# Kernel optimization log

Measured on AMD Instinct MI355X. Metric: run time of the kernel, lower is better.

Reference implementation:

```python
import jax, jax.numpy as jnp
import numpy as np

T, B, D = 1024, 64, 256   # time, batch, input dim
L, DC = 1024, 256         # context length, context dim
H, A = 256, 256           # hidden, attention dim
NEG = -1e9


def setup_inputs() -> dict:
    key = jax.random.key(0)
    ks = jax.random.split(key, 12)
    s = lambda fan: 1.0 / np.sqrt(fan)
    inp = {
        'x': jax.random.normal(ks[0], (T, B, D), jnp.float32),
        'lengths': jnp.maximum(jax.random.randint(ks[1], (B,), 1, T + 1), 1).astype(jnp.int32),
        'context': jax.random.normal(ks[2], (B, L, DC), jnp.float32),
        'ctx_lengths': jnp.maximum(jax.random.randint(ks[3], (B,), 1, L + 1), 1).astype(jnp.int32),
        'Wc': jax.random.normal(ks[4], (DC, A), jnp.float32) * s(DC),
        'Wx': jax.random.normal(ks[5], (D, A), jnp.float32) * s(D),
        'Wh': jax.random.normal(ks[6], (H, A), jnp.float32) * s(H),
        'v': jax.random.normal(ks[7], (A,), jnp.float32) * s(A),
        'W_ih': jax.random.normal(ks[8], (D + DC, 3 * H), jnp.float32) * s(D + DC),
        'W_hh': jax.random.normal(ks[9], (H, 3 * H), jnp.float32) * s(H),
        'b_ih': jnp.zeros((3 * H,), jnp.float32),
        'b_hh': jnp.zeros((3 * H,), jnp.float32),
    }
    return inp


def reference(x, lengths, context, ctx_lengths, Wc, Wx, Wh, v, W_ih, W_hh, b_ih, b_hh):
    # Precompute context projection once (shared across all timesteps). [B, L, A]
    ctx_proj = jnp.einsum('bld,da->bla', context, Wc)
    ctx_mask = jnp.arange(L)[None, :] < ctx_lengths[:, None]  # [B, L]
    h0 = jnp.zeros((B, H), x.dtype)

    def step(h, inputs):
        xt, t = inputs  # xt: [B, D]
        # Additive attention over the context.
        e = jnp.tanh(ctx_proj + (xt @ Wx)[:, None, :] + (h @ Wh)[:, None, :])  # [B, L, A]
        scores = jnp.where(ctx_mask, jnp.einsum('bla,a->bl', e, v), NEG)
        alpha = jax.nn.softmax(scores, axis=-1)                  # [B, L]
        c = jnp.einsum('bl,bld->bd', alpha, context)             # [B, DC]
        # GRU over [x_t ; c_t].
        z = jnp.concatenate([xt, c], axis=-1)                    # [B, D+DC]
        gi = z @ W_ih + b_ih
        gh = h @ W_hh + b_hh
        r = jax.nn.sigmoid(gi[:, :H] + gh[:, :H])
        u = jax.nn.sigmoid(gi[:, H:2 * H] + gh[:, H:2 * H])
        n = jnp.tanh(gi[:, 2 * H:] + r * gh[:, 2 * H:])
        h_new = u * h + (1.0 - u) * n
        valid = (t < lengths)[:, None]                           # ragged masking
        h_next = jnp.where(valid, h_new, h)
        out = jnp.where(valid, h_new, 0.0)
        return h_next, out

    h_final, outputs = jax.lax.scan(step, h0, (x, jnp.arange(T)))
    return outputs, h_final[None]  # [T, B, H], [num_layers=1, B, H]
```

## Files before the change

### kernel.cpp

```cpp
#include <hip/hip_runtime.h>
#include <cstddef>

#define T_ 1024
#define B_ 64
#define D_ 256
#define L_ 1024
#define DC_ 256
#define H_ 256
#define A_ 256
#define G3 768
#define LQ 256
#define NBLK 4

typedef unsigned int uint2v __attribute__((ext_vector_type(2)));
typedef float float4v __attribute__((ext_vector_type(4)));
typedef float float2v __attribute__((ext_vector_type(2)));

__device__ __forceinline__ float bflo(unsigned int w) { return __uint_as_float(w << 16); }
__device__ __forceinline__ float bfhi(unsigned int w) { return __uint_as_float(w & 0xffff0000u); }
__device__ __forceinline__ unsigned short f2bf(float f) {
  unsigned int x = __float_as_uint(f);
  return (unsigned short)((x + 0x7fffu + ((x >> 16) & 1u)) >> 16);
}
__device__ __forceinline__ unsigned int packbf(float lo, float hi) {
  return (unsigned int)f2bf(lo) | ((unsigned int)f2bf(hi) << 16);
}
__device__ __forceinline__ float fast_tanh(float xx) {
  float e = __expf(2.0f * xx);
  return 1.0f - 2.0f / (e + 1.0f);
}
__device__ __forceinline__ float sigmoidf_(float xx) {
  return 1.0f / (1.0f + __expf(-xx));
}
__device__ __forceinline__ void st_agent_f(float* p, float v) {
  __hip_atomic_store(p, v, __ATOMIC_RELAXED, __HIP_MEMORY_SCOPE_AGENT);
}
__device__ __forceinline__ float ld_agent_f(const float* p) {
  return __hip_atomic_load(p, __ATOMIC_RELAXED, __HIP_MEMORY_SCOPE_AGENT);
}
__device__ __forceinline__ void group_arrive(unsigned int* ctrb) {
  __syncthreads();
  if (threadIdx.x == 0) {
    __hip_atomic_fetch_add(ctrb, 1u, __ATOMIC_RELAXED, __HIP_MEMORY_SCOPE_AGENT);
  }
}
__device__ __forceinline__ void group_wait(unsigned int* ctrb, unsigned int target) {
  if (threadIdx.x == 0) {
    while (__hip_atomic_load(ctrb, __ATOMIC_RELAXED, __HIP_MEMORY_SCOPE_AGENT) < target) {
      __builtin_amdgcn_s_sleep(2);
    }
  }
  __syncthreads();
}

__global__ void f2bf_kernel(const float* __restrict__ src,
                            unsigned short* __restrict__ dst, int n) {
  int i = (blockIdx.x * blockDim.x + threadIdx.x) * 4;
  if (i < n) {
    float4 v = *(const float4*)(src + i);
    ushort4 o;
    o.x = f2bf(v.x); o.y = f2bf(v.y); o.z = f2bf(v.z); o.w = f2bf(v.w);
    *(ushort4*)(dst + i) = o;
  }
}

__global__ void pack_wih_kernel(const float* __restrict__ W_ih,
                                unsigned short* __restrict__ dst) {
  int idx = blockIdx.x * 256 + threadIdx.x;
  int kb = idx / (512 * 192);
  int rem = idx % (512 * 192);
  int r = rem / 192, jg = rem % 192;
  int g = jg >> 6, jj = jg & 63;
  int j = g * 256 + kb * 64 + jj;
  dst[idx] = f2bf(W_ih[(size_t)r * G3 + j]);
}
__global__ void pack_whh_kernel(const float* __restrict__ W_hh,
                                unsigned short* __restrict__ dst) {
  int idx = blockIdx.x * 256 + threadIdx.x;
  int kb = idx / (256 * 192);
  int rem = idx % (256 * 192);
  int r = rem / 192, jg = rem % 192;
  int g = jg >> 6, jj = jg & 63;
  int j = g * 256 + kb * 64 + jj;
  dst[idx] = f2bf(W_hh[(size_t)r * G3 + j]);
}

__global__ void ctx_proj_kernel(const float* __restrict__ context,
                                const float* __restrict__ Wc,
                                unsigned short* __restrict__ ctxT) {
  __shared__ float cs[4352];
  const int bid = blockIdx.x;
  const int b = bid >> 6;
  const int l0 = (bid & 63) << 4;
  const int tid = threadIdx.x;
  for (int idx = tid; idx < 16 * DC_; idx += 256) {
    int r = idx >> 8;
    int d = idx & 255;
    cs[r * DC_ + d] = context[((size_t)b * L_ + (l0 + r)) * DC_ + d];
  }
  __syncthreads();
  const int a = tid;
  float acc[16];
#pragma unroll
  for (int r = 0; r < 16; ++r) acc[r] = 0.0f;
  for (int d = 0; d < DC_; ++d) {
    float w = Wc[d * A_ + a];
#pragma unroll
    for (int r = 0; r < 16; ++r) acc[r] += cs[r * DC_ + d] * w;
  }
  __syncthreads();
#pragma unroll
  for (int r = 0; r < 16; ++r) cs[a * 17 + r] = acc[r];
  __syncthreads();
  for (int idx = tid; idx < 16 * A_; idx += 256) {
    int aa = idx >> 4;
    int r = idx & 15;
    ctxT[((size_t)b * A_ + aa) * L_ + l0 + r] = f2bf(cs[aa * 17 + r]);
  }
}

__global__ __launch_bounds__(1024) void encoder_kernel(
    const float* __restrict__ x, const int* __restrict__ lengths,
    const float* __restrict__ context, const int* __restrict__ ctx_lengths,
    const unsigned short* __restrict__ wx_b, const unsigned short* __restrict__ wh_b,
    const float* __restrict__ v,
    const unsigned short* __restrict__ wih_pk, const unsigned short* __restrict__ whh_pk,
    const float* __restrict__ b_ih, const float* __restrict__ b_hh,
    const unsigned short* __restrict__ ctxT, float* __restrict__ out,
    float* __restrict__ cpart, float* __restrict__ hx, unsigned int* __restrict__ ctr) {
  __shared__ __align__(16) unsigned short ctx_lds[A_ * LQ];
  __shared__ __align__(16) float scratch[4096];
  __shared__ __align__(16) float xt_s[D_];
  __shared__ __align__(16) float h_s[H_];
  __shared__ __align__(16) float c_s[DC_];
  __shared__ float2 qv_s[A_];
  __shared__ float pv_s[LQ];
  __shared__ float gatI[192], gatH[192];
  __shared__ float bsl_i[192], bsl_h[192];
  __shared__ float wsum_l[4];

  const int gb = blockIdx.x;
  const int b = gb >> 2, kb = gb & 3;
  const int tid = threadIdx.x;
  const int len = lengths[b];
  const int clen = ctx_lengths[b];
  const int lbase = kb * LQ;
  const unsigned short* ctxTb = ctxT + (size_t)b * A_ * L_;
  const float* ctxb = context + (size_t)b * L_ * DC_;
  const unsigned short* wihp = wih_pk + (size_t)kb * (512 * 192);
  const unsigned short* whhp = whh_pk + (size_t)kb * (256 * 192);
  float* cpart_grp = cpart + (size_t)b * NBLK * 264;
  float* cpart_my = cpart_grp + kb * 264;
  float* hx_b = hx + (size_t)b * 256;
  unsigned int* ctr_b = ctr + b * 32;

  const int p16 = tid >> 6, i64 = tid & 63;
  const int pq = tid / 96, jc = tid % 96;

  if (tid < 256) { h_s[tid] = 0.0f; qv_s[tid] = make_float2(0.0f, v[tid]); }
  if (tid < 192) {
    int g = tid >> 6, jj = tid & 63;
    int j = g * 256 + kb * 64 + jj;
    bsl_i[tid] = b_ih[j]; bsl_h[tid] = b_hh[j];
  }
  for (int idx = tid; idx < 16384; idx += 1024) {
    int a = idx >> 6;
    int lq = idx & 63;
    *(uint2v*)&ctx_lds[a * LQ + lq * 4] =
        *(const uint2v*)(ctxTb + (size_t)a * L_ + lbase + lq * 4);
  }
  uint2v creg[16];
#pragma unroll
  for (int i = 0; i < 16; ++i) {
    float4v cv = *(const float4v*)&ctxb[(size_t)(lbase + p16 * 16 + i) * DC_ + i64 * 4];
    creg[i].x = packbf(cv.x, cv.y);
    creg[i].y = packbf(cv.z, cv.w);
  }
  __syncthreads();

  for (int t = 0; t < len; ++t) {
    if (tid < 64) {
      *(float4v*)&xt_s[tid * 4] =
          *(const float4v*)&x[((size_t)t * B_ + b) * D_ + tid * 4];
    }
    __syncthreads();

    {
      const int a0 = i64 * 4, k0 = p16 * 16;
      float4v acc = {0.f, 0.f, 0.f, 0.f};
#pragma unroll
      for (int k = k0; k < k0 + 16; ++k) {
        float xv = xt_s[k];
        uint2v w = *(const uint2v*)(wx_b + (size_t)k * A_ + a0);
        acc.x += xv * bflo(w.x); acc.y += xv * bfhi(w.x);
        acc.z += xv * bflo(w.y); acc.w += xv * bfhi(w.y);
      }
#pragma unroll
      for (int k = k0; k < k0 + 16; ++k) {
        float hv = h_s[k];
        uint2v w = *(const uint2v*)(wh_b + (size_t)k * A_ + a0);
        acc.x += hv * bflo(w.x); acc.y += hv * bfhi(w.x);
        acc.z += hv * bflo(w.y); acc.w += hv * bfhi(w.y);
      }
      *(float4v*)&scratch[tid * 4] = acc;
    }
    __syncthreads();
    if (tid < 256) {
      float q = 0.f;
#pragma unroll
      for (int p = 0; p < 16; ++p) q += scratch[p * 256 + tid];
      qv_s[tid].x = q;
    }
    __syncthreads();

    {
      const int ll0 = i64 * 4;
      float4v acc = {0.f, 0.f, 0.f, 0.f};
      if (lbase + ll0 < clen) {
        const unsigned short* basep = ctx_lds + p16 * 16 * LQ + ll0;
#pragma unroll 4
        for (int aa = 0; aa < 16; ++aa) {
          uint2v w = *(const uint2v*)(basep + aa * LQ);
          float2 qv = qv_s[p16 * 16 + aa];
          acc.x += qv.y * fast_tanh(bflo(w.x) + qv.x);
          acc.y += qv.y * fast_tanh(bfhi(w.x) + qv.x);
          acc.z += qv.y * fast_tanh(bflo(w.y) + qv.x);
          acc.w += qv.y * fast_tanh(bfhi(w.y) + qv.x);
        }
      }
      *(float4v*)&scratch[tid * 4] = acc;
    }
    __syncthreads();
    if (tid < 256) {
      float s = 0.f;
#pragma unroll
      for (int p = 0; p < 16; ++p) s += scratch[p * 256 + tid];
      int lg = lbase + tid;
      float e = (lg < clen) ? __expf(s) : 0.f;
      pv_s[tid] = e;
      float sm = e;
#pragma unroll
      for (int off = 32; off; off >>= 1) sm += __shfl_xor(sm, off);
      if ((tid & 63) == 0) wsum_l[tid >> 6] = sm;
    }
    __syncthreads();

    {
      float4v acc = {0.f, 0.f, 0.f, 0.f};
#pragma unroll
      for (int i = 0; i < 16; ++i) {
        float pv = pv_s[p16 * 16 + i];
        uint2v w = creg[i];
        acc.x += pv * bflo(w.x); acc.y += pv * bfhi(w.x);
        acc.z += pv * bflo(w.y); acc.w += pv * bfhi(w.y);
      }
      *(float4v*)&scratch[tid * 4] = acc;
    }
    __syncthreads();
    if (tid < 256) {
      float cp = 0.f;
#pragma unroll
      for (int p = 0; p < 16; ++p) cp += scratch[p * 256 + tid];
      st_agent_f(&cpart_my[tid], cp);
    }
    if (tid == 0) {
      st_agent_f(&cpart_my[256], wsum_l[0] + wsum_l[1] + wsum_l[2] + wsum_l[3]);
    }
    group_arrive(ctr_b);

    if (tid < 768) {
      const int r0 = pq * 32;
      float a0 = 0.f, a1 = 0.f, h0 = 0.f, h1 = 0.f;
#pragma unroll 8
      for (int i = 0; i < 32; ++i) {
        float zk = xt_s[r0 + i];
        unsigned int wi = *(const unsigned int*)(wihp + (size_t)(r0 + i) * 192 + 2 * jc);
        a0 += zk * bflo(wi); a1 += zk * bfhi(wi);
        float hv = h_s[r0 + i];
        unsigned int wh = *(const unsigned int*)(whhp + (size_t)(r0 + i) * 192 + 2 * jc);
        h0 += hv * bflo(wh); h1 += hv * bfhi(wh);
      }
      *(float2v*)&scratch[pq * 192 + 2 * jc] = float2v{a0, a1};
      *(float2v*)&scratch[1536 + pq * 192 + 2 * jc] = float2v{h0, h1};
    }
    __syncthreads();
    if (tid < 192) {
      float gi = bsl_i[tid], gh = bsl_h[tid];
#pragma unroll
      for (int p = 0; p < 8; ++p) {
        gi += scratch[p * 192 + tid];
        gh += scratch[1536 + p * 192 + tid];
      }
      gatI[tid] = gi; gatH[tid] = gh;
    }
    group_wait(ctr_b, 8u * t + 4u);

    {
      float cc = 0.f;
      if (tid < 256) {
#pragma unroll
        for (int k2 = 0; k2 < 4; ++k2) cc += ld_agent_f(cpart_grp + k2 * 264 + tid);
      } else if (tid < 260) {
        wsum_l[tid - 256] = ld_agent_f(cpart_grp + (tid - 256) * 264 + 256);
      }
      __syncthreads();
      if (tid < 256) {
        c_s[tid] = cc / (wsum_l[0] + wsum_l[1] + wsum_l[2] + wsum_l[3]);
      }
    }
    __syncthreads();

    if (tid < 768) {
      const int r0 = pq * 32;
      float b0 = 0.f, b1 = 0.f;
#pragma unroll 8
      for (int i = 0; i < 32; ++i) {
        float zk = c_s[r0 + i];
        unsigned int wi =
            *(const unsigned int*)(wihp + (size_t)(256 + r0 + i) * 192 + 2 * jc);
        b0 += zk * bflo(wi); b1 += zk * bfhi(wi);
      }
      *(float2v*)&scratch[pq * 192 + 2 * jc] = float2v{b0, b1};
    }
    __syncthreads();
    if (tid < 192) {
      float gi = gatI[tid];
#pragma unroll
      for (int p = 0; p < 8; ++p) gi += scratch[p * 192 + tid];
      gatI[tid] = gi;
    }
    __syncthreads();
    if (tid < 64) {
      float r = sigmoidf_(gatI[tid] + gatH[tid]);
      float u = sigmoidf_(gatI[64 + tid] + gatH[64 + tid]);
      float n = fast_tanh(gatI[128 + tid] + r * gatH[128 + tid]);
      float hn = u * h_s[kb * 64 + tid] + (1.0f - u) * n;
      st_agent_f(&hx_b[kb * 64 + tid], hn);
      __builtin_nontemporal_store(hn, &out[((size_t)t * B_ + b) * H_ + kb * 64 + tid]);
    }
    group_arrive(ctr_b);
    group_wait(ctr_b, 8u * t + 8u);
    if (tid < 256) h_s[tid] = ld_agent_f(&hx_b[tid]);
    __syncthreads();
  }

  {
    const int n = (T_ - len) * 64;
    for (int idx = tid; idx < n; idx += 1024) {
      int tt = len + (idx >> 6);
      int ii = idx & 63;
      __builtin_nontemporal_store(0.0f, &out[((size_t)tt * B_ + b) * H_ + kb * 64 + ii]);
    }
  }
  if (tid < 64) {
    out[(size_t)T_ * B_ * H_ + (size_t)b * H_ + kb * 64 + tid] = h_s[kb * 64 + tid];
  }
}

extern "C" void kernel_launch(void* const* d_in, const int* in_sizes, int n_in,
                              void* d_out, int out_size, void* d_ws, size_t ws_size,
                              hipStream_t stream) {
  const float* x = (const float*)d_in[0];
  const int* lengths = (const int*)d_in[1];
  const float* context = (const float*)d_in[2];
  const int* ctx_lengths = (const int*)d_in[3];
  const float* Wc = (const float*)d_in[4];
  const float* Wx = (const float*)d_in[5];
  const float* Wh = (const float*)d_in[6];
  const float* v = (const float*)d_in[7];
  const float* W_ih = (const float*)d_in[8];
  const float* W_hh = (const float*)d_in[9];
  const float* b_ih = (const float*)d_in[10];
  const float* b_hh = (const float*)d_in[11];
  float* out = (float*)d_out;

  char* w = (char*)d_ws;
  unsigned short* ctxT = (unsigned short*)w;
  unsigned short* wx_b = (unsigned short*)(w + 33554432);
  unsigned short* wh_b = (unsigned short*)(w + 33685504);
  unsigned short* wih_pk = (unsigned short*)(w + 33816576);
  unsigned short* whh_pk = (unsigned short*)(w + 34603008);
  float* cpart = (float*)(w + 34996224);
  float* hx = (float*)(w + 35266560);
  unsigned int* ctr = (unsigned int*)(w + 35332096);

  hipMemsetAsync(ctr, 0, 8192, stream);
  hipLaunchKernelGGL(f2bf_kernel, dim3(64), dim3(256), 0, stream, Wx, wx_b, D_ * A_);
  hipLaunchKernelGGL(f2bf_kernel, dim3(64), dim3(256), 0, stream, Wh, wh_b, H_ * A_);
  hipLaunchKernelGGL(pack_wih_kernel, dim3(1536), dim3(256), 0, stream, W_ih, wih_pk);
  hipLaunchKernelGGL(pack_whh_kernel, dim3(768), dim3(256), 0, stream, W_hh, whh_pk);
  hipLaunchKernelGGL(ctx_proj_kernel, dim3(B_ * (L_ / 16)), dim3(256), 0, stream,
                     context, Wc, ctxT);
  hipLaunchKernelGGL(encoder_kernel, dim3(B_ * NBLK), dim3(1024), 0, stream,
                     x, lengths, context, ctx_lengths, wx_b, wh_b, v,
                     wih_pk, whh_pk, b_ih, b_hh, ctxT, out, cpart, hx, ctr);
}
```

Baseline: 56.10 ms.

## Split each batch row across eight 512-thread blocks with atomic context reduction

Changes the persistent encoder from 4 blocks of 1024 threads per batch row to 8 blocks of 512 threads, each owning 128 context positions and 32 hidden units. Partial context vectors and softmax sums are now combined with agent-scope float atomic adds into double-buffered accumulators, which are zeroed for the next step, instead of per-block partial stores followed by a 4-way gather. h is exchanged with 64-bit loads. The intent is to use more CUs and shorten per-step serial work. In exchange there are more blocks per barrier, more atomic traffic, and float atomics make the summation order nondeterministic.

After: 72.58 ms. +29.4%, slower.

```diff
diff --git a/kernel.cpp b/kernel.cpp
--- a/kernel.cpp
+++ b/kernel.cpp
@@ -9,12 +9,11 @@
 #define H_ 256
 #define A_ 256
 #define G3 768
-#define LQ 256
-#define NBLK 4
+#define LQ 128
+#define NBLK 8
 
 typedef unsigned int uint2v __attribute__((ext_vector_type(2)));
 typedef float float4v __attribute__((ext_vector_type(4)));
-typedef float float2v __attribute__((ext_vector_type(2)));
 
 __device__ __forceinline__ float bflo(unsigned int w) { return __uint_as_float(w << 16); }
 __device__ __forceinline__ float bfhi(unsigned int w) { return __uint_as_float(w & 0xffff0000u); }
@@ -37,6 +36,15 @@
 }
 __device__ __forceinline__ float ld_agent_f(const float* p) {
   return __hip_atomic_load(p, __ATOMIC_RELAXED, __HIP_MEMORY_SCOPE_AGENT);
+}
+__device__ __forceinline__ void st_agent_u64(unsigned long long* p, unsigned long long v) {
+  __hip_atomic_store(p, v, __ATOMIC_RELAXED, __HIP_MEMORY_SCOPE_AGENT);
+}
+__device__ __forceinline__ unsigned long long ld_agent_u64(const unsigned long long* p) {
+  return __hip_atomic_load(p, __ATOMIC_RELAXED, __HIP_MEMORY_SCOPE_AGENT);
+}
+__device__ __forceinline__ void add_agent_f(float* p, float v) {
+  __hip_atomic_fetch_add(p, v, __ATOMIC_RELAXED, __HIP_MEMORY_SCOPE_AGENT);
 }
 __device__ __forceinline__ void group_arrive(unsigned int* ctrb) {
   __syncthreads();
@@ -64,24 +72,24 @@
   }
 }
 
-__global__ void pack_wih_kernel(const float* __restrict__ W_ih,
-                                unsigned short* __restrict__ dst) {
+__global__ void pack_wihp_kernel(const float* __restrict__ W_ih,
+                                 unsigned short* __restrict__ dst) {
   int idx = blockIdx.x * 256 + threadIdx.x;
-  int kb = idx / (512 * 192);
-  int rem = idx % (512 * 192);
-  int r = rem / 192, jg = rem % 192;
-  int g = jg >> 6, jj = jg & 63;
-  int j = g * 256 + kb * 64 + jj;
+  int kb = idx / (512 * 96);
+  int rem = idx % (512 * 96);
+  int r = rem / 96, cj = rem % 96;
+  int g = cj >> 5, jj = cj & 31;
+  int j = g * 256 + kb * 32 + jj;
   dst[idx] = f2bf(W_ih[(size_t)r * G3 + j]);
 }
-__global__ void pack_whh_kernel(const float* __restrict__ W_hh,
-                                unsigned short* __restrict__ dst) {
+__global__ void pack_whhp_kernel(const float* __restrict__ W_hh,
+                                 unsigned short* __restrict__ dst) {
   int idx = blockIdx.x * 256 + threadIdx.x;
-  int kb = idx / (256 * 192);
-  int rem = idx % (256 * 192);
-  int r = rem / 192, jg = rem % 192;
-  int g = jg >> 6, jj = jg & 63;
-  int j = g * 256 + kb * 64 + jj;
+  int kb = idx / (256 * 96);
+  int rem = idx % (256 * 96);
+  int r = rem / 96, cj = rem % 96;
+  int g = cj >> 5, jj = cj & 31;
+  int j = g * 256 + kb * 32 + jj;
   dst[idx] = f2bf(W_hh[(size_t)r * G3 + j]);
 }
 
@@ -119,66 +127,70 @@
   }
 }
 
-__global__ __launch_bounds__(1024) void encoder_kernel(
+__global__ __launch_bounds__(512, 4) void encoder_kernel(
     const float* __restrict__ x, const int* __restrict__ lengths,
     const float* __restrict__ context, const int* __restrict__ ctx_lengths,
     const unsigned short* __restrict__ wx_b, const unsigned short* __restrict__ wh_b,
     const float* __restrict__ v,
-    const unsigned short* __restrict__ wih_pk, const unsigned short* __restrict__ whh_pk,
+    const unsigned short* __restrict__ wihp, const unsigned short* __restrict__ whhp,
     const float* __restrict__ b_ih, const float* __restrict__ b_hh,
     const unsigned short* __restrict__ ctxT, float* __restrict__ out,
-    float* __restrict__ cpart, float* __restrict__ hx, unsigned int* __restrict__ ctr) {
+    float* __restrict__ cadd, float* __restrict__ hx, unsigned int* __restrict__ ctr) {
   __shared__ __align__(16) unsigned short ctx_lds[A_ * LQ];
-  __shared__ __align__(16) float scratch[4096];
+  __shared__ __align__(16) float scratch[2048];
   __shared__ __align__(16) float xt_s[D_];
   __shared__ __align__(16) float h_s[H_];
   __shared__ __align__(16) float c_s[DC_];
-  __shared__ float2 qv_s[A_];
+  __shared__ float q_s[A_];
   __shared__ float pv_s[LQ];
-  __shared__ float gatI[192], gatH[192];
-  __shared__ float bsl_i[192], bsl_h[192];
-  __shared__ float wsum_l[4];
+  __shared__ float gatI[96], gatH[96];
 
   const int gb = blockIdx.x;
-  const int b = gb >> 2, kb = gb & 3;
+  const int b = gb >> 3, kb = gb & 7;
   const int tid = threadIdx.x;
   const int len = lengths[b];
   const int clen = ctx_lengths[b];
   const int lbase = kb * LQ;
   const unsigned short* ctxTb = ctxT + (size_t)b * A_ * L_;
   const float* ctxb = context + (size_t)b * L_ * DC_;
-  const unsigned short* wihp = wih_pk + (size_t)kb * (512 * 192);
-  const unsigned short* whhp = whh_pk + (size_t)kb * (256 * 192);
-  float* cpart_grp = cpart + (size_t)b * NBLK * 264;
-  float* cpart_my = cpart_grp + kb * 264;
+  const unsigned short* wihpk = wihp + (size_t)kb * (512 * 96);
+  const unsigned short* whhpk = whhp + (size_t)kb * (256 * 96);
   float* hx_b = hx + (size_t)b * 256;
   unsigned int* ctr_b = ctr + b * 32;
 
-  const int p16 = tid >> 6, i64 = tid & 63;
-  const int pq = tid / 96, jc = tid % 96;
-
-  if (tid < 256) { h_s[tid] = 0.0f; qv_s[tid] = make_float2(0.0f, v[tid]); }
-  if (tid < 192) {
-    int g = tid >> 6, jj = tid & 63;
-    int j = g * 256 + kb * 64 + jj;
-    bsl_i[tid] = b_ih[j]; bsl_h[tid] = b_hh[j];
-  }
-  for (int idx = tid; idx < 16384; idx += 1024) {
-    int a = idx >> 6;
-    int lq = idx & 63;
+  const int p8 = tid >> 6, i64 = tid & 63;
+  const int p16s = tid >> 5, i32 = tid & 31;
+  const int pq = tid / 48, jp = tid % 48;
+
+  if (tid < 256) { h_s[tid] = 0.0f; q_s[tid] = 0.0f; }
+  float vreg[16];
+#pragma unroll
+  for (int i = 0; i < 16; ++i) vreg[i] = v[p16s * 16 + i];
+  float breg_i = 0.f, breg_h = 0.f;
+  if (tid < 96) {
+    int j = (tid >> 5) * 256 + kb * 32 + (tid & 31);
+    breg_i = b_ih[j]; breg_h = b_hh[j];
+  }
+  for (int idx = tid; idx < 8192; idx += 512) {
+    int a = idx >> 5;
+    int lq = idx & 31;
     *(uint2v*)&ctx_lds[a * LQ + lq * 4] =
         *(const uint2v*)(ctxTb + (size_t)a * L_ + lbase + lq * 4);
   }
   uint2v creg[16];
 #pragma unroll
   for (int i = 0; i < 16; ++i) {
-    float4v cv = *(const float4v*)&ctxb[(size_t)(lbase + p16 * 16 + i) * DC_ + i64 * 4];
+    float4v cv = *(const float4v*)&ctxb[(size_t)(lbase + p8 * 16 + i) * DC_ + i64 * 4];
     creg[i].x = packbf(cv.x, cv.y);
     creg[i].y = packbf(cv.z, cv.w);
   }
   __syncthreads();
 
   for (int t = 0; t < len; ++t) {
+    const int par = t & 1;
+    float* caddb = cadd + ((size_t)(par * 64 + b)) * 288;
+    float* cshadow = cadd + ((size_t)((1 - par) * 64 + b)) * 288;
+
     if (tid < 64) {
       *(float4v*)&xt_s[tid * 4] =
           *(const float4v*)&x[((size_t)t * B_ + b) * D_ + tid * 4];
@@ -186,17 +198,17 @@
     __syncthreads();
 
     {
-      const int a0 = i64 * 4, k0 = p16 * 16;
+      const int a0 = i64 * 4, k0 = p8 * 32;
       float4v acc = {0.f, 0.f, 0.f, 0.f};
 #pragma unroll
-      for (int k = k0; k < k0 + 16; ++k) {
+      for (int k = k0; k < k0 + 32; ++k) {
         float xv = xt_s[k];
         uint2v w = *(const uint2v*)(wx_b + (size_t)k * A_ + a0);
         acc.x += xv * bflo(w.x); acc.y += xv * bfhi(w.x);
         acc.z += xv * bflo(w.y); acc.w += xv * bfhi(w.y);
       }
 #pragma unroll
-      for (int k = k0; k < k0 + 16; ++k) {
+      for (int k = k0; k < k0 + 32; ++k) {
         float hv = h_s[k];
         uint2v w = *(const uint2v*)(wh_b + (size_t)k * A_ + a0);
         acc.x += hv * bflo(w.x); acc.y += hv * bfhi(w.x);
@@ -208,40 +220,40 @@
     if (tid < 256) {
       float q = 0.f;
 #pragma unroll
-      for (int p = 0; p < 16; ++p) q += scratch[p * 256 + tid];
-      qv_s[tid].x = q;
+      for (int p = 0; p < 8; ++p) q += scratch[p * 256 + tid];
+      q_s[tid] = q;
     }
     __syncthreads();
 
     {
-      const int ll0 = i64 * 4;
+      const int l0 = i32 * 4;
       float4v acc = {0.f, 0.f, 0.f, 0.f};
-      if (lbase + ll0 < clen) {
-        const unsigned short* basep = ctx_lds + p16 * 16 * LQ + ll0;
+      if (lbase + l0 < clen) {
+        const unsigned short* basep = ctx_lds + p16s * 16 * LQ + l0;
 #pragma unroll 4
         for (int aa = 0; aa < 16; ++aa) {
           uint2v w = *(const uint2v*)(basep + aa * LQ);
-          float2 qv = qv_s[p16 * 16 + aa];
-          acc.x += qv.y * fast_tanh(bflo(w.x) + qv.x);
-          acc.y += qv.y * fast_tanh(bfhi(w.x) + qv.x);
-          acc.z += qv.y * fast_tanh(bflo(w.y) + qv.x);
-          acc.w += qv.y * fast_tanh(bfhi(w.y) + qv.x);
+          float q = q_s[p16s * 16 + aa];
+          float vv = vreg[aa];
+          acc.x += vv * fast_tanh(bflo(w.x) + q);
+          acc.y += vv * fast_tanh(bfhi(w.x) + q);
+          acc.z += vv * fast_tanh(bflo(w.y) + q);
+          acc.w += vv * fast_tanh(bfhi(w.y) + q);
         }
       }
       *(float4v*)&scratch[tid * 4] = acc;
     }
     __syncthreads();
-    if (tid < 256) {
+    if (tid < 128) {
       float s = 0.f;
 #pragma unroll
-      for (int p = 0; p < 16; ++p) s += scratch[p * 256 + tid];
-      int lg = lbase + tid;
-      float e = (lg < clen) ? __expf(s) : 0.f;
+      for (int p = 0; p < 16; ++p) s += scratch[p * 128 + tid];
+      float e = (lbase + tid < clen) ? __expf(s) : 0.f;
       pv_s[tid] = e;
       float sm = e;
 #pragma unroll
       for (int off = 32; off; off >>= 1) sm += __shfl_xor(sm, off);
-      if ((tid & 63) == 0) wsum_l[tid >> 6] = sm;
+      if ((tid & 63) == 0) add_agent_f(caddb + 256, sm);
     }
     __syncthreads();
 
@@ -249,7 +261,7 @@
       float4v acc = {0.f, 0.f, 0.f, 0.f};
 #pragma unroll
       for (int i = 0; i < 16; ++i) {
-        float pv = pv_s[p16 * 16 + i];
+        float pv = pv_s[p8 * 16 + i];
         uint2v w = creg[i];
         acc.x += pv * bflo(w.x); acc.y += pv * bfhi(w.x);
         acc.z += pv * bflo(w.y); acc.w += pv * bfhi(w.y);
@@ -260,100 +272,101 @@
     if (tid < 256) {
       float cp = 0.f;
 #pragma unroll
-      for (int p = 0; p < 16; ++p) cp += scratch[p * 256 + tid];
-      st_agent_f(&cpart_my[tid], cp);
-    }
-    if (tid == 0) {
-      st_agent_f(&cpart_my[256], wsum_l[0] + wsum_l[1] + wsum_l[2] + wsum_l[3]);
+      for (int p = 0; p < 8; ++p) cp += scratch[p * 256 + tid];
+      add_agent_f(caddb + tid, cp);
     }
     group_arrive(ctr_b);
 
-    if (tid < 768) {
+    if (tid < 384) {
       const int r0 = pq * 32;
       float a0 = 0.f, a1 = 0.f, h0 = 0.f, h1 = 0.f;
 #pragma unroll 8
       for (int i = 0; i < 32; ++i) {
         float zk = xt_s[r0 + i];
-        unsigned int wi = *(const unsigned int*)(wihp + (size_t)(r0 + i) * 192 + 2 * jc);
+        unsigned int wi = *(const unsigned int*)(wihpk + (size_t)(r0 + i) * 96 + 2 * jp);
         a0 += zk * bflo(wi); a1 += zk * bfhi(wi);
         float hv = h_s[r0 + i];
-        unsigned int wh = *(const unsigned int*)(whhp + (size_t)(r0 + i) * 192 + 2 * jc);
+        unsigned int wh = *(const unsigned int*)(whhpk + (size_t)(r0 + i) * 96 + 2 * jp);
         h0 += hv * bflo(wh); h1 += hv * bfhi(wh);
       }
-      *(float2v*)&scratch[pq * 192 + 2 * jc] = float2v{a0, a1};
-      *(float2v*)&scratch[1536 + pq * 192 + 2 * jc] = float2v{h0, h1};
-    }
-    __syncthreads();
-    if (tid < 192) {
-      float gi = bsl_i[tid], gh = bsl_h[tid];
+      scratch[pq * 96 + 2 * jp] = a0; scratch[pq * 96 + 2 * jp + 1] = a1;
+      scratch[768 + pq * 96 + 2 * jp] = h0; scratch[768 + pq * 96 + 2 * jp + 1] = h1;
+    }
+    __syncthreads();
+    if (tid < 96) {
+      float gi = breg_i, gh = breg_h;
 #pragma unroll
       for (int p = 0; p < 8; ++p) {
-        gi += scratch[p * 192 + tid];
-        gh += scratch[1536 + p * 192 + tid];
+        gi += scratch[p * 96 + tid];
+        gh += scratch[768 + p * 96 + tid];
       }
       gatI[tid] = gi; gatH[tid] = gh;
     }
-    group_wait(ctr_b, 8u * t + 4u);
+    group_wait(ctr_b, 16u * t + 8u);
 
     {
-      float cc = 0.f;
-      if (tid < 256) {
-#pragma unroll
-        for (int k2 = 0; k2 < 4; ++k2) cc += ld_agent_f(cpart_grp + k2 * 264 + tid);
-      } else if (tid < 260) {
-        wsum_l[tid - 256] = ld_agent_f(cpart_grp + (tid - 256) * 264 + 256);
-      }
+      unsigned long long cc = 0;
+      if (tid < 128) cc = ld_agent_u64((const unsigned long long*)caddb + tid);
+      if (tid == 128) pv_s[0] = ld_agent_f(caddb + 256);
       __syncthreads();
-      if (tid < 256) {
-        c_s[tid] = cc / (wsum_l[0] + wsum_l[1] + wsum_l[2] + wsum_l[3]);
-      }
-    }
-    __syncthreads();
-
-    if (tid < 768) {
+      if (tid < 128) {
+        float inv = 1.0f / pv_s[0];
+        c_s[2 * tid] = __uint_as_float((unsigned int)cc) * inv;
+        c_s[2 * tid + 1] = __uint_as_float((unsigned int)(cc >> 32)) * inv;
+      }
+      if (tid < 16) st_agent_u64((unsigned long long*)(cshadow + kb * 32) + tid, 0ull);
+      if (tid == 16 && kb == 0) st_agent_f(cshadow + 256, 0.0f);
+    }
+    __syncthreads();
+
+    if (tid < 384) {
       const int r0 = pq * 32;
       float b0 = 0.f, b1 = 0.f;
 #pragma unroll 8
       for (int i = 0; i < 32; ++i) {
         float zk = c_s[r0 + i];
         unsigned int wi =
-            *(const unsigned int*)(wihp + (size_t)(256 + r0 + i) * 192 + 2 * jc);
+            *(const unsigned int*)(wihpk + (size_t)(256 + r0 + i) * 96 + 2 * jp);
         b0 += zk * bflo(wi); b1 += zk * bfhi(wi);
       }
-      *(float2v*)&scratch[pq * 192 + 2 * jc] = float2v{b0, b1};
-    }
-    __syncthreads();
-    if (tid < 192) {
+      scratch[pq * 96 + 2 * jp] = b0; scratch[pq * 96 + 2 * jp + 1] = b1;
+    }
+    __syncthreads();
+    if (tid < 96) {
       float gi = gatI[tid];
 #pragma unroll
-      for (int p = 0; p < 8; ++p) gi += scratch[p * 192 + tid];
+      for (int p = 0; p < 8; ++p) gi += scratch[p * 96 + tid];
       gatI[tid] = gi;
     }
     __syncthreads();
-    if (tid < 64) {
+    if (tid < 32) {
       float r = sigmoidf_(gatI[tid] + gatH[tid]);
-      float u = sigmoidf_(gatI[64 + tid] + gatH[64 + tid]);
-      float n = fast_tanh(gatI[128 + tid] + r * gatH[128 + tid]);
-      float hn = u * h_s[kb * 64 + tid] + (1.0f - u) * n;
-      st_agent_f(&hx_b[kb * 64 + tid], hn);
-      __builtin_nontemporal_store(hn, &out[((size_t)t * B_ + b) * H_ + kb * 64 + tid]);
+      float u = sigmoidf_(gatI[32 + tid] + gatH[32 + tid]);
+      float n = fast_tanh(gatI[64 + tid] + r * gatH[64 + tid]);
+      float hn = u * h_s[kb * 32 + tid] + (1.0f - u) * n;
+      st_agent_f(&hx_b[kb * 32 + tid], hn);
+      __builtin_nontemporal_store(hn, &out[((size_t)t * B_ + b) * H_ + kb * 32 + tid]);
     }
     group_arrive(ctr_b);
-    group_wait(ctr_b, 8u * t + 8u);
-    if (tid < 256) h_s[tid] = ld_agent_f(&hx_b[tid]);
+    group_wait(ctr_b, 16u * t + 16u);
+    if (tid < 128) {
+      unsigned long long hh = ld_agent_u64((const unsigned long long*)hx_b + tid);
+      h_s[2 * tid] = __uint_as_float((unsigned int)hh);
+      h_s[2 * tid + 1] = __uint_as_float((unsigned int)(hh >> 32));
+    }
     __syncthreads();
   }
 
   {
-    const int n = (T_ - len) * 64;
-    for (int idx = tid; idx < n; idx += 1024) {
-      int tt = len + (idx >> 6);
-      int ii = idx & 63;
-      __builtin_nontemporal_store(0.0f, &out[((size_t)tt * B_ + b) * H_ + kb * 64 + ii]);
-    }
-  }
-  if (tid < 64) {
-    out[(size_t)T_ * B_ * H_ + (size_t)b * H_ + kb * 64 + tid] = h_s[kb * 64 + tid];
+    const int n = (T_ - len) * 32;
+    for (int idx = tid; idx < n; idx += 512) {
+      int tt = len + (idx >> 5);
+      int ii = idx & 31;
+      __builtin_nontemporal_store(0.0f, &out[((size_t)tt * B_ + b) * H_ + kb * 32 + ii]);
+    }
+  }
+  if (tid < 32) {
+    out[(size_t)T_ * B_ * H_ + (size_t)b * H_ + kb * 32 + tid] = h_s[kb * 32 + tid];
   }
 }
 
@@ -378,20 +391,20 @@
   unsigned short* ctxT = (unsigned short*)w;
   unsigned short* wx_b = (unsigned short*)(w + 33554432);
   unsigned short* wh_b = (unsigned short*)(w + 33685504);
-  unsigned short* wih_pk = (unsigned short*)(w + 33816576);
-  unsigned short* whh_pk = (unsigned short*)(w + 34603008);
-  float* cpart = (float*)(w + 34996224);
-  float* hx = (float*)(w + 35266560);
-  unsigned int* ctr = (unsigned int*)(w + 35332096);
-
-  hipMemsetAsync(ctr, 0, 8192, stream);
+  unsigned short* wihp = (unsigned short*)(w + 33816576);
+  unsigned short* whhp = (unsigned short*)(w + 34603008);
+  float* hx = (float*)(w + 34996224);
+  unsigned int* ctr = (unsigned int*)(w + 35061760);
+  float* cadd = (float*)(w + 35069952);
+
+  hipMemsetAsync(w + 35061760, 0, 8192 + 147456, stream);
   hipLaunchKernelGGL(f2bf_kernel, dim3(64), dim3(256), 0, stream, Wx, wx_b, D_ * A_);
   hipLaunchKernelGGL(f2bf_kernel, dim3(64), dim3(256), 0, stream, Wh, wh_b, H_ * A_);
-  hipLaunchKernelGGL(pack_wih_kernel, dim3(1536), dim3(256), 0, stream, W_ih, wih_pk);
-  hipLaunchKernelGGL(pack_whh_kernel, dim3(768), dim3(256), 0, stream, W_hh, whh_pk);
+  hipLaunchKernelGGL(pack_wihp_kernel, dim3(1536), dim3(256), 0, stream, W_ih, wihp);
+  hipLaunchKernelGGL(pack_whhp_kernel, dim3(768), dim3(256), 0, stream, W_hh, whhp);
   hipLaunchKernelGGL(ctx_proj_kernel, dim3(B_ * (L_ / 16)), dim3(256), 0, stream,
                      context, Wc, ctxT);
-  hipLaunchKernelGGL(encoder_kernel, dim3(B_ * NBLK), dim3(1024), 0, stream,
+  hipLaunchKernelGGL(encoder_kernel, dim3(B_ * NBLK), dim3(512), 0, stream,
                      x, lengths, context, ctx_lengths, wx_b, wh_b, v,
-                     wih_pk, whh_pk, b_ih, b_hh, ctxT, out, cpart, hx, ctr);
-}
+                     wihp, whhp, b_ih, b_hh, ctxT, out, cadd, hx, ctr);
+}
```

## Fuse context projection into encoder prologue and stream bf16 context per step

Applied to the files above, without the earlier changes.

Drops the separate ctx_proj kernel and computes the context projection directly into LDS inside the encoder kernel's prologue. It also stops holding the bf16 context slice in registers across the time loop. Instead, a new f2bf kernel writes a bf16 copy of context to global memory, and each step reloads its slice from there. The aim is to cut register pressure and a kernel launch plus its global round trip. The cost is extra global or L2 reads on every timestep, plus a serial prologue projection spread over only 256 blocks.

New measurement: 54.64 ms. 2.6% less time.

```diff
diff --git a/kernel.cpp b/kernel.cpp
--- a/kernel.cpp
+++ b/kernel.cpp
@@ -15,15 +15,13 @@
 typedef unsigned int uint2v __attribute__((ext_vector_type(2)));
 typedef float float4v __attribute__((ext_vector_type(4)));
 typedef float float2v __attribute__((ext_vector_type(2)));
+typedef unsigned short ushort4v __attribute__((ext_vector_type(4)));
 
 __device__ __forceinline__ float bflo(unsigned int w) { return __uint_as_float(w << 16); }
 __device__ __forceinline__ float bfhi(unsigned int w) { return __uint_as_float(w & 0xffff0000u); }
 __device__ __forceinline__ unsigned short f2bf(float f) {
   unsigned int x = __float_as_uint(f);
   return (unsigned short)((x + 0x7fffu + ((x >> 16) & 1u)) >> 16);
-}
-__device__ __forceinline__ unsigned int packbf(float lo, float hi) {
-  return (unsigned int)f2bf(lo) | ((unsigned int)f2bf(hi) << 16);
 }
 __device__ __forceinline__ float fast_tanh(float xx) {
   float e = __expf(2.0f * xx);
@@ -85,48 +83,15 @@
   dst[idx] = f2bf(W_hh[(size_t)r * G3 + j]);
 }
 
-__global__ void ctx_proj_kernel(const float* __restrict__ context,
-                                const float* __restrict__ Wc,
-                                unsigned short* __restrict__ ctxT) {
-  __shared__ float cs[4352];
-  const int bid = blockIdx.x;
-  const int b = bid >> 6;
-  const int l0 = (bid & 63) << 4;
-  const int tid = threadIdx.x;
-  for (int idx = tid; idx < 16 * DC_; idx += 256) {
-    int r = idx >> 8;
-    int d = idx & 255;
-    cs[r * DC_ + d] = context[((size_t)b * L_ + (l0 + r)) * DC_ + d];
-  }
-  __syncthreads();
-  const int a = tid;
-  float acc[16];
-#pragma unroll
-  for (int r = 0; r < 16; ++r) acc[r] = 0.0f;
-  for (int d = 0; d < DC_; ++d) {
-    float w = Wc[d * A_ + a];
-#pragma unroll
-    for (int r = 0; r < 16; ++r) acc[r] += cs[r * DC_ + d] * w;
-  }
-  __syncthreads();
-#pragma unroll
-  for (int r = 0; r < 16; ++r) cs[a * 17 + r] = acc[r];
-  __syncthreads();
-  for (int idx = tid; idx < 16 * A_; idx += 256) {
-    int aa = idx >> 4;
-    int r = idx & 15;
-    ctxT[((size_t)b * A_ + aa) * L_ + l0 + r] = f2bf(cs[aa * 17 + r]);
-  }
-}
-
 __global__ __launch_bounds__(1024) void encoder_kernel(
     const float* __restrict__ x, const int* __restrict__ lengths,
     const float* __restrict__ context, const int* __restrict__ ctx_lengths,
+    const float* __restrict__ Wc,
     const unsigned short* __restrict__ wx_b, const unsigned short* __restrict__ wh_b,
     const float* __restrict__ v,
     const unsigned short* __restrict__ wih_pk, const unsigned short* __restrict__ whh_pk,
     const float* __restrict__ b_ih, const float* __restrict__ b_hh,
-    const unsigned short* __restrict__ ctxT, float* __restrict__ out,
+    const unsigned short* __restrict__ ctx_bf, float* __restrict__ out,
     float* __restrict__ cpart, float* __restrict__ hx, unsigned int* __restrict__ ctr) {
   __shared__ __align__(16) unsigned short ctx_lds[A_ * LQ];
   __shared__ __align__(16) float scratch[4096];
@@ -145,8 +110,8 @@
   const int len = lengths[b];
   const int clen = ctx_lengths[b];
   const int lbase = kb * LQ;
-  const unsigned short* ctxTb = ctxT + (size_t)b * A_ * L_;
   const float* ctxb = context + (size_t)b * L_ * DC_;
+  const unsigned short* ctxbf_b = ctx_bf + (size_t)b * L_ * DC_;
   const unsigned short* wihp = wih_pk + (size_t)kb * (512 * 192);
   const unsigned short* whhp = whh_pk + (size_t)kb * (256 * 192);
   float* cpart_grp = cpart + (size_t)b * NBLK * 264;
@@ -163,20 +128,29 @@
     int j = g * 256 + kb * 64 + jj;
     bsl_i[tid] = b_ih[j]; bsl_h[tid] = b_hh[j];
   }
-  for (int idx = tid; idx < 16384; idx += 1024) {
-    int a = idx >> 6;
-    int lq = idx & 63;
-    *(uint2v*)&ctx_lds[a * LQ + lq * 4] =
-        *(const uint2v*)(ctxTb + (size_t)a * L_ + lbase + lq * 4);
-  }
-  uint2v creg[16];
-#pragma unroll
-  for (int i = 0; i < 16; ++i) {
-    float4v cv = *(const float4v*)&ctxb[(size_t)(lbase + p16 * 16 + i) * DC_ + i64 * 4];
-    creg[i].x = packbf(cv.x, cv.y);
-    creg[i].y = packbf(cv.z, cv.w);
-  }
   __syncthreads();
+
+  {
+    const int a = tid & 255, lq4 = tid >> 8;
+    for (int tl = 0; tl < 16; ++tl) {
+      for (int idx = tid; idx < 4096; idx += 1024) {
+        int r = idx >> 8, d = idx & 255;
+        scratch[d * 16 + r] = ctxb[(size_t)(lbase + tl * 16 + r) * DC_ + d];
+      }
+      __syncthreads();
+      float a0 = 0.f, a1 = 0.f, a2 = 0.f, a3 = 0.f;
+#pragma unroll 4
+      for (int d = 0; d < 256; ++d) {
+        float w = Wc[(size_t)d * A_ + a];
+        const float* ps = &scratch[d * 16 + lq4 * 4];
+        a0 += ps[0] * w; a1 += ps[1] * w; a2 += ps[2] * w; a3 += ps[3] * w;
+      }
+      int l0 = tl * 16 + lq4 * 4;
+      ushort4v o; o.x = f2bf(a0); o.y = f2bf(a1); o.z = f2bf(a2); o.w = f2bf(a3);
+      *(ushort4v*)&ctx_lds[a * LQ + l0] = o;
+      __syncthreads();
+    }
+  }
 
   for (int t = 0; t < len; ++t) {
     if (tid < 64) {
@@ -212,6 +186,12 @@
       qv_s[tid].x = q;
     }
     __syncthreads();
+
+    uint2v cstage[16];
+#pragma unroll
+    for (int i = 0; i < 16; ++i) {
+      cstage[i] = *(const uint2v*)(ctxbf_b + (size_t)(lbase + p16 * 16 + i) * DC_ + i64 * 4);
+    }
 
     {
       const int ll0 = i64 * 4;
@@ -250,7 +230,7 @@
 #pragma unroll
       for (int i = 0; i < 16; ++i) {
         float pv = pv_s[p16 * 16 + i];
-        uint2v w = creg[i];
+        uint2v w = cstage[i];
         acc.x += pv * bflo(w.x); acc.y += pv * bfhi(w.x);
         acc.z += pv * bflo(w.y); acc.w += pv * bfhi(w.y);
       }
@@ -375,7 +355,7 @@
   float* out = (float*)d_out;
 
   char* w = (char*)d_ws;
-  unsigned short* ctxT = (unsigned short*)w;
+  unsigned short* ctx_bf = (unsigned short*)w;
   unsigned short* wx_b = (unsigned short*)(w + 33554432);
   unsigned short* wh_b = (unsigned short*)(w + 33685504);
   unsigned short* wih_pk = (unsigned short*)(w + 33816576);
@@ -385,13 +365,13 @@
   unsigned int* ctr = (unsigned int*)(w + 35332096);
 
   hipMemsetAsync(ctr, 0, 8192, stream);
+  hipLaunchKernelGGL(f2bf_kernel, dim3(16384), dim3(256), 0, stream,
+                     context, ctx_bf, B_ * L_ * DC_);
   hipLaunchKernelGGL(f2bf_kernel, dim3(64), dim3(256), 0, stream, Wx, wx_b, D_ * A_);
   hipLaunchKernelGGL(f2bf_kernel, dim3(64), dim3(256), 0, stream, Wh, wh_b, H_ * A_);
   hipLaunchKernelGGL(pack_wih_kernel, dim3(1536), dim3(256), 0, stream, W_ih, wih_pk);
   hipLaunchKernelGGL(pack_whh_kernel, dim3(768), dim3(256), 0, stream, W_hh, whh_pk);
-  hipLaunchKernelGGL(ctx_proj_kernel, dim3(B_ * (L_ / 16)), dim3(256), 0, stream,
-                     context, Wc, ctxT);
   hipLaunchKernelGGL(encoder_kernel, dim3(B_ * NBLK), dim3(1024), 0, stream,
-                     x, lengths, context, ctx_lengths, wx_b, wh_b, v,
-                     wih_pk, whh_pk, b_ih, b_hh, ctxT, out, cpart, hx, ctr);
-}
+                     x, lengths, context, ctx_lengths, Wc, wx_b, wh_b, v,
+                     wih_pk, whh_pk, b_ih, b_hh, ctx_bf, out, cpart, hx, ctr);
+}
```
